# Kernel tuning notes

Measured on AMD Instinct MI355X. Metric: run time of the kernel, lower is better.

Reference implementation:

```python
import jax, jax.numpy as jnp
import numpy as np

E = 256; H = 8; HD = E // H
L_LEN = 300; A_LEN = 250
T = 768; B = 4
NEG = -1e9


def setup_inputs() -> dict:
    rng = jax.random.key(0)
    ks = jax.random.split(rng, 16)
    n = lambda k, s, sc=1.0: jax.random.normal(k, s, dtype=jnp.float32) * sc
    return {
        "query": n(ks[0], (T, B, E)),
        "key": n(ks[1], (T, B, E)),
        "value": n(ks[2], (T, B, E)),
        "in_proj_w": n(ks[3], (3 * E, E), 0.05),
        "in_proj_b": jnp.zeros((3 * E,), jnp.float32),
        "out_w": n(ks[4], (7, E, E), 0.05),
        "out_b": jnp.zeros((7, E), jnp.float32),
        "s_l_w": n(ks[5], (E, 4 * E), 0.05),
        "s_l_b": jnp.zeros((E,), jnp.float32),
        "s_a_w": n(ks[6], (E, 4 * E), 0.05),
        "s_a_b": jnp.zeros((E,), jnp.float32),
        "s_v_w": n(ks[7], (E, 4 * E), 0.05),
        "s_v_b": jnp.zeros((E,), jnp.float32),
        "final_w": n(ks[8], (E, E), 0.05),
        "final_b": jnp.zeros((E,), jnp.float32),
    }


def _forward(query, key, value, in_proj_w, in_proj_b, out_w, out_b,
             s_l_w, s_l_b, s_a_w, s_a_b, s_v_w, s_v_b, final_w, final_b):
    t, b, e = query.shape
    scaling = HD ** -0.5
    Wq, Wk, Wv = in_proj_w[:E], in_proj_w[E:2 * E], in_proj_w[2 * E:]
    bq, bk, bv = in_proj_b[:E], in_proj_b[E:2 * E], in_proj_b[2 * E:]
    q = (query @ Wq.T + bq) * scaling
    k = key @ Wk.T + bk
    v = value @ Wv.T + bv
    # (T, B, E) -> (B*H, T, HD)
    sh = lambda x: x.reshape(t, b * H, HD).transpose(1, 0, 2)
    q, k, v = sh(q), sh(k), sh(v)
    # shared QK^T, reused by all 7 masked branches
    scores = jnp.einsum('bth,bsh->bts', q, k)  # (B*H, T, T)
    idx = jnp.arange(t)
    seg = jnp.where(idx < L_LEN, 0, jnp.where(idx < L_LEN + A_LEN, 1, 2))

    def branch(i, mods):
        # m[j] = 1 iff position j belongs to one of the selected modalities
        m = sum((seg == s) for s in mods).astype(scores.dtype)  # (T,)
        # additive mask: in-set query attends only in-set keys; out-of-set
        # query rows get all -1e9 (uniform softmax, zeroed by row mask below)
        add = jnp.where((m[:, None] * m[None, :]) > 0, 0.0, NEG)
        w = jax.nn.softmax(scores + add, axis=-1) * m[None, :, None]
        o = jnp.einsum('bts,bsh->bth', w, v * m[None, :, None])
        o = o.transpose(1, 0, 2).reshape(t, b, e)
        return o @ out_w[i].T + out_b[i]

    attn_lav = branch(0, (0, 1, 2))
    attn_la = branch(1, (0, 1))
    attn_lv = branch(2, (0, 2))
    attn_av = branch(3, (1, 2))
    attn_l = branch(4, (0,))
    attn_a = branch(5, (1,))
    attn_v = branch(6, (2,))

    sl = jnp.concatenate([attn_lav, attn_la, attn_lv, attn_l], -1) @ s_l_w.T + s_l_b
    sa = jnp.concatenate([attn_lav, attn_la, attn_av, attn_a], -1) @ s_a_w.T + s_a_b
    sv = jnp.concatenate([attn_lav, attn_lv, attn_av, attn_v], -1) @ s_v_w.T + s_v_b
    return (sl + sa + sv) @ final_w.T + final_b


def reference(query, key, value, in_proj_w, in_proj_b, out_w, out_b,
              s_l_w, s_l_b, s_a_w, s_a_b, s_v_w, s_v_b, final_w, final_b):
    return _forward(query, key, value, in_proj_w, in_proj_b, out_w, out_b,
                    s_l_w, s_l_b, s_a_w, s_a_b, s_v_w, s_v_b, final_w, final_b)
```

## Files before the change

### kernel.cpp

```cpp
#include <hip/hip_runtime.h>
#include <hip/hip_bf16.h>

#define E 256
#define H 8
#define HD 32
#define T 768
#define B 4
#define BH 32

typedef __attribute__((ext_vector_type(8))) short bf16x8;
typedef __attribute__((ext_vector_type(4))) float f32x4;

__device__ __forceinline__ float b2f(__hip_bfloat16 x) { return __bfloat162float(x); }

__device__ __forceinline__ unsigned short f2bf_u(float x) {
    __hip_bfloat16 h = __float2bfloat16(x);
    return *(unsigned short*)&h;
}
__device__ __forceinline__ float bfu2f(unsigned short u) {
    return __uint_as_float(((unsigned int)u) << 16);
}

__device__ __forceinline__ void f8_split(const float* v, bf16x8& h, bf16x8& l) {
    #pragma unroll
    for (int e = 0; e < 8; ++e) {
        unsigned short hu = f2bf_u(v[e]);
        h[e] = (short)hu;
        l[e] = (short)f2bf_u(v[e] - bfu2f(hu));
    }
}

#define MFMA3(ACC, AH, AL, BH_, BL_)                                         \
    ACC = __builtin_amdgcn_mfma_f32_16x16x32_bf16(AH, BH_, ACC, 0, 0, 0);    \
    ACC = __builtin_amdgcn_mfma_f32_16x16x32_bf16(AH, BL_, ACC, 0, 0, 0);    \
    ACC = __builtin_amdgcn_mfma_f32_16x16x32_bf16(AL, BH_, ACC, 0, 0, 0);

__device__ __forceinline__ float ldu(const void* p, size_t i, int f32) {
    if (f32) return ((const float*)p)[i];
    return b2f(((const __hip_bfloat16*)p)[i]);
}

__device__ __forceinline__ float gsum_load(int i, int r2, int r,
                                           const void* sl, const void* sa,
                                           const void* sv, int f32)
{
    size_t base = (size_t)r2 * 1024;
    switch (i) {
        case 0: return ldu(sl, base + r, f32) + ldu(sa, base + r, f32) + ldu(sv, base + r, f32);
        case 1: return ldu(sl, base + 256 + r, f32) + ldu(sa, base + 256 + r, f32);
        case 2: return ldu(sl, base + 512 + r, f32) + ldu(sv, base + 256 + r, f32);
        case 3: return ldu(sa, base + 512 + r, f32) + ldu(sv, base + 512 + r, f32);
        case 4: return ldu(sl, base + 768 + r, f32);
        case 5: return ldu(sa, base + 768 + r, f32);
        default: return ldu(sv, base + 768 + r, f32);
    }
}

__global__ void detect_kernel(const unsigned short* __restrict__ q,
                              int* __restrict__ flag) {
    if (threadIdx.x == 0 && blockIdx.x == 0) {
        int f32 = 0;
        for (int i = 0; i < 256; ++i) {
            unsigned int bits = ((unsigned int)q[i]) << 16;
            float v = __uint_as_float(bits);
            if (!(v == v) || fabsf(v) > 1e4f) f32 = 1;
        }
        *flag = f32;
    }
}

__global__ __launch_bounds__(256) void conv_kernel(
    const void* query, const void* key, const void* value, const void* w,
    const void* sl, const void* sa, const void* sv, const void* outw,
    const int* __restrict__ flag,
    unsigned short* __restrict__ XFh, unsigned short* __restrict__ XFl,
    unsigned short* __restrict__ WFh, unsigned short* __restrict__ WFl,
    unsigned short* __restrict__ GFh, unsigned short* __restrict__ GFl,
    unsigned short* __restrict__ OWFh, unsigned short* __restrict__ OWFl)
{
    int f32 = *flag;
    int item = blockIdx.x * 256 + threadIdx.x;
    if (item < 294912) {
        int inp = item / 98304;
        int rem = item % 98304;
        int row = rem >> 5, kg = rem & 31;
        const void* X = (inp == 0) ? query : (inp == 1) ? key : value;
        float v[8];
        if (f32) {
            const float4* p = (const float4*)((const float*)X +
                               (size_t)row * 256 + kg * 8);
            *(float4*)&v[0] = p[0];
            *(float4*)&v[4] = p[1];
        } else {
            #pragma unroll
            for (int j = 0; j < 8; ++j)
                v[j] = ldu(X, (size_t)row * 256 + kg * 8 + j, 0);
        }
        bf16x8 h, l;
        f8_split(v, h, l);
        int rb = row >> 4, kb = kg >> 2;
        int lane = (row & 15) | ((kg & 3) << 4);
        size_t idx = (((size_t)(inp * 192 + rb) * 8 + kb) * 64 + lane) * 8;
        *(bf16x8*)&XFh[idx] = h;
        *(bf16x8*)&XFl[idx] = l;
    } else if (item < 319488) {
        int rem = item - 294912;
        int gc = rem >> 5, kg = rem & 31;
        float v[8];
        if (f32) {
            const float4* p = (const float4*)((const float*)w +
                               (size_t)gc * 256 + kg * 8);
            *(float4*)&v[0] = p[0];
            *(float4*)&v[4] = p[1];
        } else {
            #pragma unroll
            for (int j = 0; j < 8; ++j)
                v[j] = ldu(w, (size_t)gc * 256 + kg * 8 + j, 0);
        }
        bf16x8 h, l;
        f8_split(v, h, l);
        int sec = gc >> 8, c = gc & 255;
        int cb = c >> 4, kb = kg >> 2;
        int lane = (c & 15) | ((kg & 3) << 4);
        size_t idx = (((size_t)(sec * 16 + cb) * 8 + kb) * 64 + lane) * 8;
        *(bf16x8*)&WFh[idx] = h;
        *(bf16x8*)&WFl[idx] = l;
    } else if (item < 376832) {
        int rem = item - 319488;
        int i = rem >> 13;
        int rest = rem & 8191;
        int r2 = rest >> 5, kg = rest & 31;
        float v[8];
        #pragma unroll
        for (int j = 0; j < 8; ++j)
            v[j] = gsum_load(i, r2, kg * 8 + j, sl, sa, sv, f32);
        bf16x8 h, l;
        f8_split(v, h, l);
        int rb = r2 >> 4, kb = kg >> 2;
        int lane = (r2 & 15) | ((kg & 3) << 4);
        size_t idx = (((size_t)(i * 16 + rb) * 8 + kb) * 64 + lane) * 8;
        *(bf16x8*)&GFh[idx] = h;
        *(bf16x8*)&GFl[idx] = l;
    } else if (item < 434176) {
        int rem = item - 376832;
        int i = rem >> 13;
        int rest = rem & 8191;
        int kg = rest >> 8, c = rest & 255;
        float v[8];
        #pragma unroll
        for (int j = 0; j < 8; ++j)
            v[j] = ldu(outw, (size_t)i * 65536 + (kg * 8 + j) * 256 + c, f32);
        bf16x8 h, l;
        f8_split(v, h, l);
        int cb = c >> 4, kb = kg >> 2;
        int lane = (c & 15) | ((kg & 3) << 4);
        size_t idx = (((size_t)(i * 16 + cb) * 8 + kb) * 64 + lane) * 8;
        *(bf16x8*)&OWFh[idx] = h;
        *(bf16x8*)&OWFl[idx] = l;
    }
}

__global__ __launch_bounds__(256) void qkv_mfma_kernel(
    const unsigned short* __restrict__ XFh, const unsigned short* __restrict__ XFl,
    const unsigned short* __restrict__ WFh, const unsigned short* __restrict__ WFl,
    const void* bias, const int* __restrict__ flag,
    float* __restrict__ qws,
    unsigned short* __restrict__ KGh, unsigned short* __restrict__ KGl,
    unsigned short* __restrict__ VGh, unsigned short* __restrict__ VGl)
{
    int f32 = *flag;
    int bx = blockIdx.x;
    int rb = blockIdx.y;
    int sec = bx >> 2, cg = bx & 3;
    int w = threadIdx.x >> 6, lane = threadIdx.x & 63;
    int m = lane & 15, quad = lane >> 4;
    int cb = cg * 4 + w;

    const unsigned short* Ah = XFh + (((size_t)(sec * 192 + rb) * 8) * 64 + lane) * 8;
    const unsigned short* Al = XFl + (((size_t)(sec * 192 + rb) * 8) * 64 + lane) * 8;
    const unsigned short* Bh = WFh + (((size_t)(sec * 16 + cb) * 8) * 64 + lane) * 8;
    const unsigned short* Bl = WFl + (((size_t)(sec * 16 + cb) * 8) * 64 + lane) * 8;

    f32x4 acc = {};
    #pragma unroll
    for (int kb = 0; kb < 8; ++kb) {
        size_t off = (size_t)kb * 512;
        bf16x8 ah = *(const bf16x8*)(Ah + off);
        bf16x8 al = *(const bf16x8*)(Al + off);
        bf16x8 bh = *(const bf16x8*)(Bh + off);
        bf16x8 bl = *(const bf16x8*)(Bl + off);
        MFMA3(acc, ah, al, bh, bl)
    }

    int c_local = cb * 16 + m;
    float bv = ldu(bias, sec * 256 + c_local, f32);
    int h = c_local >> 5, hd = c_local & 31;

    if (sec == 0) {
        #pragma unroll
        for (int rr = 0; rr < 4; ++rr) {
            int row = rb * 16 + quad * 4 + rr;
            int t = row >> 2, b = row & 3;
            float val = (acc[rr] + bv) * 0.17677669529663687f;
            qws[((size_t)((b * H + h) * T + t)) * HD + hd] = val;
        }
    } else if (sec == 1) {
        #pragma unroll
        for (int rr = 0; rr < 4; ++rr) {
            int row = rb * 16 + quad * 4 + rr;
            int s = row >> 2, b = row & 3;
            int bh_ = b * 8 + h, ch = s >> 6;
            float val = acc[rr] + bv;
            unsigned short hu = f2bf_u(val);
            unsigned short lu = f2bf_u(val - bfu2f(hu));
            size_t bi = (((size_t)(bh_ * 12 + ch) * 4 + ((s >> 4) & 3)) * 64
                         + ((s & 15) | ((hd >> 3) << 4))) * 8 + (hd & 7);
            KGh[bi] = hu;
            KGl[bi] = lu;
        }
    } else {
        #pragma unroll
        for (int rr = 0; rr < 4; ++rr) {
            int row = rb * 16 + quad * 4 + rr;
            int s = row >> 2, b = row & 3;
            int bh_ = b * 8 + h, ch = s >> 6;
            float val = acc[rr] + bv;
            unsigned short hu = f2bf_u(val);
            unsigned short lu = f2bf_u(val - bfu2f(hu));
            int sl = s & 63, ks = sl >> 5, j = sl & 7, q3 = (sl >> 3) & 3;
            int hdb = hd >> 4;
            size_t bi = ((((size_t)(bh_ * 12 + ch) * 2 + hdb) * 2 + ks) * 64
                         + ((hd & 15) | (q3 << 4))) * 8 + j;
            VGh[bi] = hu;
            VGl[bi] = lu;
        }
    }
}

__global__ __launch_bounds__(256) void wcomb1_mfma_kernel(
    const unsigned short* __restrict__ GFh, const unsigned short* __restrict__ GFl,
    const unsigned short* __restrict__ OWFh, const unsigned short* __restrict__ OWFl,
    float* __restrict__ Mtmp)
{
    int cgrp = blockIdx.x;
    int rb   = blockIdx.y;
    int i    = blockIdx.z;
    int w = threadIdx.x >> 6, lane = threadIdx.x & 63;
    int m = lane & 15, quad = lane >> 4;
    int cb = cgrp * 4 + w;

    const unsigned short* Ah = GFh + (((size_t)(i * 16 + rb) * 8) * 64 + lane) * 8;
    const unsigned short* Al = GFl + (((size_t)(i * 16 + rb) * 8) * 64 + lane) * 8;
    const unsigned short* Bh = OWFh + (((size_t)(i * 16 + cb) * 8) * 64 + lane) * 8;
    const unsigned short* Bl = OWFl + (((size_t)(i * 16 + cb) * 8) * 64 + lane) * 8;

    f32x4 acc = {};
    #pragma unroll
    for (int kb = 0; kb < 8; ++kb) {
        size_t off = (size_t)kb * 512;
        bf16x8 ah = *(const bf16x8*)(Ah + off);
        bf16x8 al = *(const bf16x8*)(Al + off);
        bf16x8 bh = *(const bf16x8*)(Bh + off);
        bf16x8 bl = *(const bf16x8*)(Bl + off);
        MFMA3(acc, ah, al, bh, bl)
    }
    #pragma unroll
    for (int rr = 0; rr < 4; ++rr) {
        int r2 = rb * 16 + quad * 4 + rr;
        Mtmp[(size_t)i * 65536 + r2 * 256 + cb * 16 + m] = acc[rr];
    }
}

__global__ __launch_bounds__(256) void attn_mfma_kernel(
    const float* __restrict__ qws,
    const unsigned short* __restrict__ KGh, const unsigned short* __restrict__ KGl,
    const unsigned short* __restrict__ VGh, const unsigned short* __restrict__ VGl,
    unsigned short* __restrict__ Ohi, unsigned short* __restrict__ Olo)
{
    int tile = blockIdx.x;
    int bh   = blockIdx.y;
    int t0 = tile * 32;
    int tid = threadIdx.x;
    int w = tid >> 6, lane = tid & 63;
    int m = lane & 15, quad = lane >> 4;
    int tb = w & 1, hdb = w >> 1;

    __shared__ __align__(16) unsigned int EPK[2][2048];
    __shared__ float SP[4][16][3];
    float* PL = (float*)&EPK[0][0];

    bf16x8 aqh, aql;
    {
        const float* qr = qws + ((size_t)bh * T + t0 + tb * 16 + m) * HD + quad * 8;
        float qv[8];
        *(float4*)&qv[0] = *(const float4*)qr;
        *(float4*)&qv[4] = *(const float4*)(qr + 4);
        f8_split(qv, aqh, aql);
    }

    f32x4 acc0 = {}, acc1 = {}, acc2 = {};
    float ss0[4] = {}, ss1[4] = {}, ss2[4] = {};

    for (int ch = 0; ch < 12; ++ch) {
        int base = ch * 64;
        int buf = ch & 1;
        #pragma unroll
        for (int sbi = 0; sbi < 2; ++sbi) {
            int sb = (w >> 1) * 2 + sbi;
            size_t kfi = (((size_t)(bh * 12 + ch) * 4 + sb) * 64 + lane) * 8;
            bf16x8 bkh = *(const bf16x8*)(KGh + kfi);
            bf16x8 bkl = *(const bf16x8*)(KGl + kfi);
            f32x4 d = {};
            MFMA3(d, aqh, aql, bkh, bkl)
            int s64 = sb * 16 + m;
            int sglob = base + s64;
            int ksw = s64 >> 5, qp = (s64 >> 3) & 3, jp = m & 7;
            unsigned int* eb = &EPK[buf][(tb * 2 + ksw) * 512 + jp];
            #pragma unroll
            for (int r = 0; r < 4; ++r) {
                float e = __expf(d[r]);
                if (sglob < 300) ss0[r] += e;
                else if (sglob < 550) ss1[r] += e;
                else ss2[r] += e;
                unsigned short hu = f2bf_u(e);
                unsigned short lu = f2bf_u(e - bfu2f(hu));
                eb[((quad * 4 + r) + 16 * qp) * 8] =
                    (unsigned int)hu | ((unsigned int)lu << 16);
            }
        }
        __syncthreads();

        #pragma unroll
        for (int ks = 0; ks < 2; ++ks) {
            const unsigned int* ep = &EPK[buf][((tb * 2 + ks) * 64 + lane) * 8];
            uint4 p0 = *(const uint4*)ep;
            uint4 p1 = *(const uint4*)(ep + 4);
            bf16x8 aeh, ael;
            aeh[0] = (short)(p0.x & 0xffff); ael[0] = (short)(p0.x >> 16);
            aeh[1] = (short)(p0.y & 0xffff); ael[1] = (short)(p0.y >> 16);
            aeh[2] = (short)(p0.z & 0xffff); ael[2] = (short)(p0.z >> 16);
            aeh[3] = (short)(p0.w & 0xffff); ael[3] = (short)(p0.w >> 16);
            aeh[4] = (short)(p1.x & 0xffff); ael[4] = (short)(p1.x >> 16);
            aeh[5] = (short)(p1.y & 0xffff); ael[5] = (short)(p1.y >> 16);
            aeh[6] = (short)(p1.z & 0xffff); ael[6] = (short)(p1.z >> 16);
            aeh[7] = (short)(p1.w & 0xffff); ael[7] = (short)(p1.w >> 16);
            size_t vfi = ((((size_t)(bh * 12 + ch) * 2 + hdb) * 2 + ks) * 64 + lane) * 8;
            bf16x8 bvh = *(const bf16x8*)(VGh + vfi);
            bf16x8 bvl = *(const bf16x8*)(VGl + vfi);
            int s_lo = base + ks * 32;
            if (s_lo + 32 <= 300) { MFMA3(acc0, aeh, ael, bvh, bvl) }
            else if (s_lo >= 300 && s_lo + 32 <= 550) { MFMA3(acc1, aeh, ael, bvh, bvl) }
            else if (s_lo >= 550) { MFMA3(acc2, aeh, ael, bvh, bvl) }
            else {
                int bnd = (s_lo < 300) ? 300 : 550;
                bf16x8 eha = aeh, ela = ael, ehb = aeh, elb = ael;
                #pragma unroll
                for (int j = 0; j < 8; ++j) {
                    int s = s_lo + quad * 8 + j;
                    if (s < bnd) { ehb[j] = 0; elb[j] = 0; }
                    else         { eha[j] = 0; ela[j] = 0; }
                }
                if (s_lo < 300) { MFMA3(acc0, eha, ela, bvh, bvl)
                                  MFMA3(acc1, ehb, elb, bvh, bvl) }
                else            { MFMA3(acc1, eha, ela, bvh, bvl)
                                  MFMA3(acc2, ehb, elb, bvh, bvl) }
            }
        }
    }

    #pragma unroll
    for (int sg = 0; sg < 3; ++sg)
        #pragma unroll
        for (int r = 0; r < 4; ++r) {
            float v = (sg == 0) ? ss0[r] : (sg == 1) ? ss1[r] : ss2[r];
            v += __shfl_down(v, 8, 16);
            v += __shfl_down(v, 4, 16);
            v += __shfl_down(v, 2, 16);
            v += __shfl_down(v, 1, 16);
            if (m == 0) SP[w][quad * 4 + r][sg] = v;
        }
    __syncthreads();

    #pragma unroll
    for (int r = 0; r < 4; ++r) {
        int t32 = tb * 16 + quad * 4 + r;
        int hd = hdb * 16 + m;
        PL[0 * 1152 + t32 * 36 + hd] = acc0[r];
        PL[1 * 1152 + t32 * 36 + hd] = acc1[r];
        PL[2 * 1152 + t32 * 36 + hd] = acc2[r];
    }
    __syncthreads();

    int tt = tid >> 3, q4 = tid & 7;
    float Pv[3][4];
    #pragma unroll
    for (int sg = 0; sg < 3; ++sg) {
        const float4 p = *(const float4*)&PL[sg * 1152 + tt * 36 + q4 * 4];
        Pv[sg][0] = p.x; Pv[sg][1] = p.y; Pv[sg][2] = p.z; Pv[sg][3] = p.w;
    }
    int tbe = tt >> 4, t16 = tt & 15;
    float S0 = SP[tbe][t16][0] + SP[tbe + 2][t16][0];
    float S1 = SP[tbe][t16][1] + SP[tbe + 2][t16][1];
    float S2 = SP[tbe][t16][2] + SP[tbe + 2][t16][2];

    int t_glob = t0 + tt;
    int g = (t_glob < 300) ? 0 : (t_glob < 550 ? 1 : 2);
    int b_ = bh >> 3, h_ = bh & 7;
    int row = t_glob * B + b_;
    int lslot = (row & 15) + ((q4 >> 1) << 4);
    int j0 = (q4 & 1) * 4;
    size_t fbase = (((size_t)(row >> 4) * 56 + h_) * 64 + lslot) * 8 + j0;
    const int masks[7] = {7, 3, 5, 6, 1, 2, 4};
    #pragma unroll
    for (int i = 0; i < 7; ++i) {
        int mm = masks[i];
        float n0 = 0.f, n1 = 0.f, n2 = 0.f, n3 = 0.f, den = 0.f;
        if (mm & 1) { n0 += Pv[0][0]; n1 += Pv[0][1]; n2 += Pv[0][2]; n3 += Pv[0][3]; den += S0; }
        if (mm & 2) { n0 += Pv[1][0]; n1 += Pv[1][1]; n2 += Pv[1][2]; n3 += Pv[1][3]; den += S1; }
        if (mm & 4) { n0 += Pv[2][0]; n1 += Pv[2][1]; n2 += Pv[2][2]; n3 += Pv[2][3]; den += S2; }
        float r = 1.f / den;
        int live = (mm >> g) & 1;
        float o[4];
        o[0] = live ? n0 * r : 0.f;
        o[1] = live ? n1 * r : 0.f;
        o[2] = live ? n2 * r : 0.f;
        o[3] = live ? n3 * r : 0.f;
        ushort4 hi4, lo4;
        unsigned short* hp = (unsigned short*)&hi4;
        unsigned short* lp = (unsigned short*)&lo4;
        #pragma unroll
        for (int j = 0; j < 4; ++j) {
            unsigned short hu = f2bf_u(o[j]);
            hp[j] = hu;
            lp[j] = f2bf_u(o[j] - bfu2f(hu));
        }
        size_t addr = fbase + (size_t)i * (8 * 64 * 8);
        *(ushort4*)&Ohi[addr] = hi4;
        *(ushort4*)&Olo[addr] = lo4;
    }
}

__global__ __launch_bounds__(256) void wcomb2_gemm_kernel(
    const float* __restrict__ Mtmp, const void* finalw,
    const int* __restrict__ flag,
    unsigned short* __restrict__ DThi, unsigned short* __restrict__ DTlo)
{
    int f32 = *flag;
    int bx = blockIdx.x;
    int by = blockIdx.y;
    int i  = blockIdx.z;
    int tid = threadIdx.x;
    int tx = tid & 15, ty = tid >> 4;
    int colbase = bx * 32, rowbase = by * 32;
    __shared__ __align__(16) float AsT[32][34];
    __shared__ __align__(16) float Bs[32][34];
    float acc[2][2] = {};

    for (int kb = 0; kb < 8; ++kb) {
        __syncthreads();
        #pragma unroll
        for (int l = 0; l < 4; ++l) {
            int idx = l * 256 + tid;
            int c = idx & 31, kk = idx >> 5;
            AsT[kk][c] = Mtmp[(size_t)i * 65536 + (kb * 32 + kk) * 256 + rowbase + c];
            int k2 = idx & 31, n = idx >> 5;
            Bs[k2][n] = ldu(finalw, (size_t)(colbase + n) * 256 + kb * 32 + k2, f32);
        }
        __syncthreads();
        #pragma unroll 8
        for (int kk = 0; kk < 32; ++kk) {
            const float2 av = *(const float2*)&AsT[kk][ty * 2];
            const float2 bv = *(const float2*)&Bs[kk][tx * 2];
            acc[0][0] += av.x * bv.x; acc[0][1] += av.x * bv.y;
            acc[1][0] += av.y * bv.x; acc[1][1] += av.y * bv.y;
        }
    }
    #pragma unroll
    for (int u = 0; u < 2; ++u)
        #pragma unroll
        for (int v = 0; v < 2; ++v) {
            int c = rowbase + ty * 2 + u, e = colbase + tx * 2 + v;
            float a = acc[u][v];
            unsigned short hu = f2bf_u(a);
            size_t fidx = (((size_t)(e >> 4) * 56 + i * 8 + (c >> 5)) * 64
                           + (e & 15) + (((c >> 3) & 3) << 4)) * 8 + (c & 7);
            DThi[fidx] = hu;
            DTlo[fidx] = f2bf_u(a - bfu2f(hu));
        }
}

__global__ __launch_bounds__(256) void bias1_kernel(
    const void* sl, const void* sa, const void* sv, const void* outb,
    const void* slb, const void* sab, const void* svb,
    const int* __restrict__ flag, float* __restrict__ c0)
{
    int f32 = *flag;
    int r2 = blockIdx.x, m = threadIdx.x;
    __shared__ float red[256];
    float acc = 0.f;
    #pragma unroll
    for (int i = 0; i < 7; ++i)
        acc += ldu(outb, i * 256 + m, f32) * gsum_load(i, r2, m, sl, sa, sv, f32);
    red[m] = acc;
    __syncthreads();
    for (int s = 128; s > 0; s >>= 1) {
        if (m < s) red[m] += red[m + s];
        __syncthreads();
    }
    if (m == 0)
        c0[r2] = red[0] + ldu(slb, r2, f32) + ldu(sab, r2, f32) + ldu(svb, r2, f32);
}

__global__ __launch_bounds__(256) void bias2_kernel(
    const float* __restrict__ c0, const void* finalw, const void* finalb,
    const int* __restrict__ flag, float* __restrict__ d0)
{
    int f32 = *flag;
    int e = blockIdx.x, r = threadIdx.x;
    __shared__ float red[256];
    red[r] = c0[r] * ldu(finalw, (size_t)e * 256 + r, f32);
    __syncthreads();
    for (int s = 128; s > 0; s >>= 1) {
        if (r < s) red[r] += red[r + s];
        __syncthreads();
    }
    if (r == 0)
        d0[e] = red[0] + ldu(finalb, e, f32);
}

__global__ __launch_bounds__(256) void final_gemm_mfma_kernel(
    const unsigned short* __restrict__ Ohi, const unsigned short* __restrict__ Olo,
    const unsigned short* __restrict__ DThi, const unsigned short* __restrict__ DTlo,
    const float* __restrict__ d0, const int* __restrict__ flag,
    void* __restrict__ outv)
{
    int f32 = *flag;
    int bx = blockIdx.x;
    int by = blockIdx.y;
    int w  = threadIdx.x >> 6;
    int lane = threadIdx.x & 63;
    int m = lane & 15, quad = lane >> 4;
    int R0 = by * 16, C0 = bx * 64 + w * 16;

    int t0 = R0 >> 2, t1 = (R0 + 15) >> 2;
    int g0 = (t0 < 300) ? 0 : (t0 < 550 ? 1 : 2);
    int g1 = (t1 < 300) ? 0 : (t1 < 550 ? 1 : 2);
    int activeset = (1 << g0) | (1 << g1);
    const int masks[7] = {7, 3, 5, 6, 1, 2, 4};

    const unsigned short* Abase_h = Ohi + (size_t)by * 56 * 512 + lane * 8;
    const unsigned short* Abase_l = Olo + (size_t)by * 56 * 512 + lane * 8;
    const unsigned short* Bbase_h = DThi + (size_t)(bx * 4 + w) * 56 * 512 + lane * 8;
    const unsigned short* Bbase_l = DTlo + (size_t)(bx * 4 + w) * 56 * 512 + lane * 8;

    f32x4 acc = {};
    for (int i = 0; i < 7; ++i) {
        if (!(masks[i] & activeset)) continue;
        #pragma unroll
        for (int kb = 0; kb < 8; ++kb) {
            size_t off = (size_t)(i * 8 + kb) * 512;
            bf16x8 ah = *(const bf16x8*)(Abase_h + off);
            bf16x8 al = *(const bf16x8*)(Abase_l + off);
            bf16x8 bh = *(const bf16x8*)(Bbase_h + off);
            bf16x8 bl = *(const bf16x8*)(Bbase_l + off);
            acc = __builtin_amdgcn_mfma_f32_16x16x32_bf16(ah, bh, acc, 0, 0, 0);
            acc = __builtin_amdgcn_mfma_f32_16x16x32_bf16(ah, bl, acc, 0, 0, 0);
            acc = __builtin_amdgcn_mfma_f32_16x16x32_bf16(al, bh, acc, 0, 0, 0);
        }
    }
    float dv = d0[C0 + m];
    #pragma unroll
    for (int r = 0; r < 4; ++r) {
        int row = R0 + quad * 4 + r;
        int col = C0 + m;
        float val = acc[r] + dv;
        if (f32) ((float*)outv)[(size_t)row * 256 + col] = val;
        else ((__hip_bfloat16*)outv)[(size_t)row * 256 + col] = __float2bfloat16(val);
    }
}

extern "C" void kernel_launch(void* const* d_in, const int* in_sizes, int n_in,
                              void* d_out, int out_size, void* d_ws, size_t ws_size,
                              hipStream_t stream) {
    const void* query     = d_in[0];
    const void* key       = d_in[1];
    const void* value     = d_in[2];
    const void* in_proj_w = d_in[3];
    const void* in_proj_b = d_in[4];
    const void* out_w     = d_in[5];
    const void* out_b     = d_in[6];
    const void* s_l_w     = d_in[7];
    const void* s_l_b     = d_in[8];
    const void* s_a_w     = d_in[9];
    const void* s_a_b     = d_in[10];
    const void* s_v_w     = d_in[11];
    const void* s_v_b     = d_in[12];
    const void* final_w   = d_in[13];
    const void* final_b   = d_in[14];

    float* ws     = (float*)d_ws;
    float* qws    = ws;
    unsigned short* KGh = (unsigned short*)(ws + 786432);
    unsigned short* KGl = KGh + 786432;
    unsigned short* VGh = (unsigned short*)(ws + 1572864);
    unsigned short* VGl = VGh + 786432;
    unsigned short* Ohi = (unsigned short*)(ws + 2359296);
    unsigned short* Olo = (unsigned short*)(ws + 5111808);
    unsigned short* XFh = (unsigned short*)(ws + 2359296);
    unsigned short* XFl = XFh + 2359296;
    unsigned short* WFh = XFl + 2359296;
    unsigned short* WFl = WFh + 196608;
    unsigned short* GFh = (unsigned short*)(ws + 4915200);
    unsigned short* GFl = GFh + 458752;
    unsigned short* OWFh = GFl + 458752;
    unsigned short* OWFl = OWFh + 458752;
    float* Mtmp   = ws + 7864320;
    unsigned short* DThi = (unsigned short*)(ws + 8323072);
    unsigned short* DTlo = (unsigned short*)(ws + 8552448);
    float* d0     = ws + 8781824;
    int*   flag   = (int*)(ws + 8782080);
    float* c0     = Mtmp;

    detect_kernel<<<1, 64, 0, stream>>>((const unsigned short*)query, flag);
    conv_kernel<<<1696, 256, 0, stream>>>(query, key, value, in_proj_w,
                                          s_l_w, s_a_w, s_v_w, out_w, flag,
                                          XFh, XFl, WFh, WFl,
                                          GFh, GFl, OWFh, OWFl);
    qkv_mfma_kernel<<<dim3(12, 192), 256, 0, stream>>>(XFh, XFl, WFh, WFl,
                                                       in_proj_b, flag, qws,
                                                       KGh, KGl, VGh, VGl);
    wcomb1_mfma_kernel<<<dim3(4, 16, 7), 256, 0, stream>>>(GFh, GFl, OWFh, OWFl,
                                                           Mtmp);
    attn_mfma_kernel<<<dim3(24, 32), 256, 0, stream>>>(qws, KGh, KGl, VGh, VGl,
                                                       Ohi, Olo);
    wcomb2_gemm_kernel<<<dim3(8, 8, 7), 256, 0, stream>>>(Mtmp, final_w, flag,
                                                          DThi, DTlo);
    bias1_kernel<<<256, 256, 0, stream>>>(s_l_w, s_a_w, s_v_w, out_b,
                                          s_l_b, s_a_b, s_v_b, flag, c0);
    bias2_kernel<<<256, 256, 0, stream>>>(c0, final_w, final_b, flag, d0);
    final_gemm_mfma_kernel<<<dim3(4, 192), 256, 0, stream>>>(Ohi, Olo, DThi, DTlo,
                                                             d0, flag, d_out);
}
```

Measured before the change: 198.3 us.

## Split attention key loop across two blocks and combine partials in a new kernel

The attention kernel now splits its 12 key chunks into two halves across a new grid z dimension, doubling the block count from 768 to 1536 to fill more CUs. Each half writes unnormalized PV accumulators and row exp-sums to global scratch buffers. A new combine kernel sums the two partials and does the per-branch normalization and the bf16 hi/lo output packing. This trades extra global traffic and an additional launch for more parallelism. It relies on the softmax not subtracting a running max, so partial sums can be added directly.

Result: slower. 207.1 us (+4.4%).

```diff
diff --git a/kernel.cpp b/kernel.cpp
--- a/kernel.cpp
+++ b/kernel.cpp
@@ -275,10 +275,11 @@
     const float* __restrict__ qws,
     const unsigned short* __restrict__ KGh, const unsigned short* __restrict__ KGl,
     const unsigned short* __restrict__ VGh, const unsigned short* __restrict__ VGl,
-    unsigned short* __restrict__ Ohi, unsigned short* __restrict__ Olo)
+    float* __restrict__ PACC, float* __restrict__ PSUM)
 {
     int tile = blockIdx.x;
     int bh   = blockIdx.y;
+    int z    = blockIdx.z;
     int t0 = tile * 32;
     int tid = threadIdx.x;
     int w = tid >> 6, lane = tid & 63;
@@ -287,7 +288,6 @@
 
     __shared__ __align__(16) unsigned int EPK[2][2048];
     __shared__ float SP[4][16][3];
-    float* PL = (float*)&EPK[0][0];
 
     bf16x8 aqh, aql;
     {
@@ -301,7 +301,7 @@
     f32x4 acc0 = {}, acc1 = {}, acc2 = {};
     float ss0[4] = {}, ss1[4] = {}, ss2[4] = {};
 
-    for (int ch = 0; ch < 12; ++ch) {
+    for (int ch = z * 6; ch < z * 6 + 6; ++ch) {
         int base = ch * 64;
         int buf = ch & 1;
         #pragma unroll
@@ -381,29 +381,45 @@
         }
     __syncthreads();
 
+    size_t pb = ((((size_t)z * 24 + tile) * 32 + bh) * 3) * 1024;
     #pragma unroll
     for (int r = 0; r < 4; ++r) {
-        int t32 = tb * 16 + quad * 4 + r;
-        int hd = hdb * 16 + m;
-        PL[0 * 1152 + t32 * 36 + hd] = acc0[r];
-        PL[1 * 1152 + t32 * 36 + hd] = acc1[r];
-        PL[2 * 1152 + t32 * 36 + hd] = acc2[r];
-    }
-    __syncthreads();
-
+        int idx = (tb * 16 + quad * 4 + r) * 32 + hdb * 16 + m;
+        PACC[pb + idx]        = acc0[r];
+        PACC[pb + 1024 + idx] = acc1[r];
+        PACC[pb + 2048 + idx] = acc2[r];
+    }
+    if (tid < 96) {
+        int sg = tid >> 5, t32 = tid & 31;
+        int tbe = t32 >> 4, t16 = t32 & 15;
+        PSUM[(((size_t)z * 24 + tile) * 32 + bh) * 96 + sg * 32 + t32] =
+            SP[tbe][t16][sg] + SP[tbe + 2][t16][sg];
+    }
+}
+
+__global__ __launch_bounds__(256) void attn_combine_kernel(
+    const float* __restrict__ PACC, const float* __restrict__ PSUM,
+    unsigned short* __restrict__ Ohi, unsigned short* __restrict__ Olo)
+{
+    int tile = blockIdx.x;
+    int bh   = blockIdx.y;
+    int tid = threadIdx.x;
     int tt = tid >> 3, q4 = tid & 7;
-    float Pv[3][4];
+
+    size_t p0 = (((size_t)0 * 24 + tile) * 32 + bh) * 3072;
+    size_t p1 = (((size_t)1 * 24 + tile) * 32 + bh) * 3072;
+    float Pv[3][4], S[3];
     #pragma unroll
     for (int sg = 0; sg < 3; ++sg) {
-        const float4 p = *(const float4*)&PL[sg * 1152 + tt * 36 + q4 * 4];
-        Pv[sg][0] = p.x; Pv[sg][1] = p.y; Pv[sg][2] = p.z; Pv[sg][3] = p.w;
-    }
-    int tbe = tt >> 4, t16 = tt & 15;
-    float S0 = SP[tbe][t16][0] + SP[tbe + 2][t16][0];
-    float S1 = SP[tbe][t16][1] + SP[tbe + 2][t16][1];
-    float S2 = SP[tbe][t16][2] + SP[tbe + 2][t16][2];
-
-    int t_glob = t0 + tt;
+        const float4 a = *(const float4*)&PACC[p0 + sg * 1024 + tt * 32 + q4 * 4];
+        const float4 b = *(const float4*)&PACC[p1 + sg * 1024 + tt * 32 + q4 * 4];
+        Pv[sg][0] = a.x + b.x; Pv[sg][1] = a.y + b.y;
+        Pv[sg][2] = a.z + b.z; Pv[sg][3] = a.w + b.w;
+        S[sg] = PSUM[((size_t)tile * 32 + bh) * 96 + sg * 32 + tt]
+              + PSUM[((size_t)(24 + tile) * 32 + bh) * 96 + sg * 32 + tt];
+    }
+
+    int t_glob = tile * 32 + tt;
     int g = (t_glob < 300) ? 0 : (t_glob < 550 ? 1 : 2);
     int b_ = bh >> 3, h_ = bh & 7;
     int row = t_glob * B + b_;
@@ -415,9 +431,9 @@
     for (int i = 0; i < 7; ++i) {
         int mm = masks[i];
         float n0 = 0.f, n1 = 0.f, n2 = 0.f, n3 = 0.f, den = 0.f;
-        if (mm & 1) { n0 += Pv[0][0]; n1 += Pv[0][1]; n2 += Pv[0][2]; n3 += Pv[0][3]; den += S0; }
-        if (mm & 2) { n0 += Pv[1][0]; n1 += Pv[1][1]; n2 += Pv[1][2]; n3 += Pv[1][3]; den += S1; }
-        if (mm & 4) { n0 += Pv[2][0]; n1 += Pv[2][1]; n2 += Pv[2][2]; n3 += Pv[2][3]; den += S2; }
+        if (mm & 1) { n0 += Pv[0][0]; n1 += Pv[0][1]; n2 += Pv[0][2]; n3 += Pv[0][3]; den += S[0]; }
+        if (mm & 2) { n0 += Pv[1][0]; n1 += Pv[1][1]; n2 += Pv[1][2]; n3 += Pv[1][3]; den += S[1]; }
+        if (mm & 4) { n0 += Pv[2][0]; n1 += Pv[2][1]; n2 += Pv[2][2]; n3 += Pv[2][3]; den += S[2]; }
         float r = 1.f / den;
         int live = (mm >> g) & 1;
         float o[4];
@@ -620,6 +636,8 @@
     float* d0     = ws + 8781824;
     int*   flag   = (int*)(ws + 8782080);
     float* c0     = Mtmp;
+    float* PACC   = ws + 8782336;
+    float* PSUM   = ws + 13500928;
 
     detect_kernel<<<1, 64, 0, stream>>>((const unsigned short*)query, flag);
     conv_kernel<<<1696, 256, 0, stream>>>(query, key, value, in_proj_w,
@@ -631,8 +649,9 @@
                                                        KGh, KGl, VGh, VGl);
     wcomb1_mfma_kernel<<<dim3(4, 16, 7), 256, 0, stream>>>(GFh, GFl, OWFh, OWFl,
                                                            Mtmp);
-    attn_mfma_kernel<<<dim3(24, 32), 256, 0, stream>>>(qws, KGh, KGl, VGh, VGl,
-                                                       Ohi, Olo);
+    attn_mfma_kernel<<<dim3(24, 32, 2), 256, 0, stream>>>(qws, KGh, KGl, VGh, VGl,
+                                                          PACC, PSUM);
+    attn_combine_kernel<<<dim3(24, 32), 256, 0, stream>>>(PACC, PSUM, Ohi, Olo);
     wcomb2_gemm_kernel<<<dim3(8, 8, 7), 256, 0, stream>>>(Mtmp, final_w, flag,
                                                           DThi, DTlo);
     bias1_kernel<<<256, 256, 0, stream>>>(s_l_w, s_a_w, s_v_w, out_b,
```

## Prefetch next K/V chunk into registers and swizzle LDS exp buffer

Applied to the files above, without the earlier changes.

The attention kernel now loads the next chunk's K and V MFMA fragments into registers while the current chunk is computed, which hides global load latency behind the exp and MFMA work. The LDS writes and reads of the packed exp values use an XOR swizzle to reduce bank conflicts. Launch bounds now request three blocks per CU, and the chunk loop is unrolled by two. The extra prefetch registers could raise register pressure or cause spills under the occupancy hint.

Measured after the change: 194.8 us. No clear change (-1.8%).

```diff
diff --git a/kernel.cpp b/kernel.cpp
--- a/kernel.cpp
+++ b/kernel.cpp
@@ -271,7 +271,7 @@
     }
 }
 
-__global__ __launch_bounds__(256) void attn_mfma_kernel(
+__global__ __launch_bounds__(256, 3) void attn_mfma_kernel(
     const float* __restrict__ qws,
     const unsigned short* __restrict__ KGh, const unsigned short* __restrict__ KGl,
     const unsigned short* __restrict__ VGh, const unsigned short* __restrict__ VGl,
@@ -301,21 +301,44 @@
     f32x4 acc0 = {}, acc1 = {}, acc2 = {};
     float ss0[4] = {}, ss1[4] = {}, ss2[4] = {};
 
+    int sb0 = (w >> 1) * 2;
+
+    bf16x8 ckh0, ckl0, ckh1, ckl1, cvh0, cvl0, cvh1, cvl1;
+    {
+        size_t k0 = (((size_t)(bh * 12 + 0) * 4 + sb0) * 64 + lane) * 8;
+        ckh0 = *(const bf16x8*)(KGh + k0);       ckl0 = *(const bf16x8*)(KGl + k0);
+        ckh1 = *(const bf16x8*)(KGh + k0 + 512); ckl1 = *(const bf16x8*)(KGl + k0 + 512);
+        size_t v0 = ((((size_t)(bh * 12 + 0) * 2 + hdb) * 2) * 64 + lane) * 8;
+        cvh0 = *(const bf16x8*)(VGh + v0);       cvl0 = *(const bf16x8*)(VGl + v0);
+        cvh1 = *(const bf16x8*)(VGh + v0 + 512); cvl1 = *(const bf16x8*)(VGl + v0 + 512);
+    }
+
+    #pragma unroll 2
     for (int ch = 0; ch < 12; ++ch) {
         int base = ch * 64;
         int buf = ch & 1;
+
+        bf16x8 nkh0, nkl0, nkh1, nkl1, nvh0, nvl0, nvh1, nvl1;
+        if (ch < 11) {
+            size_t kn = (((size_t)(bh * 12 + ch + 1) * 4 + sb0) * 64 + lane) * 8;
+            nkh0 = *(const bf16x8*)(KGh + kn);       nkl0 = *(const bf16x8*)(KGl + kn);
+            nkh1 = *(const bf16x8*)(KGh + kn + 512); nkl1 = *(const bf16x8*)(KGl + kn + 512);
+            size_t vn = ((((size_t)(bh * 12 + ch + 1) * 2 + hdb) * 2) * 64 + lane) * 8;
+            nvh0 = *(const bf16x8*)(VGh + vn);       nvl0 = *(const bf16x8*)(VGl + vn);
+            nvh1 = *(const bf16x8*)(VGh + vn + 512); nvl1 = *(const bf16x8*)(VGl + vn + 512);
+        }
+
         #pragma unroll
         for (int sbi = 0; sbi < 2; ++sbi) {
-            int sb = (w >> 1) * 2 + sbi;
-            size_t kfi = (((size_t)(bh * 12 + ch) * 4 + sb) * 64 + lane) * 8;
-            bf16x8 bkh = *(const bf16x8*)(KGh + kfi);
-            bf16x8 bkl = *(const bf16x8*)(KGl + kfi);
+            bf16x8 bkh = sbi ? ckh1 : ckh0;
+            bf16x8 bkl = sbi ? ckl1 : ckl0;
             f32x4 d = {};
             MFMA3(d, aqh, aql, bkh, bkl)
+            int sb = sb0 + sbi;
             int s64 = sb * 16 + m;
             int sglob = base + s64;
             int ksw = s64 >> 5, qp = (s64 >> 3) & 3, jp = m & 7;
-            unsigned int* eb = &EPK[buf][(tb * 2 + ksw) * 512 + jp];
+            int wbase = (tb * 2 + ksw) * 512 + jp;
             #pragma unroll
             for (int r = 0; r < 4; ++r) {
                 float e = __expf(d[r]);
@@ -324,17 +347,21 @@
                 else ss2[r] += e;
                 unsigned short hu = f2bf_u(e);
                 unsigned short lu = f2bf_u(e - bfu2f(hu));
-                eb[((quad * 4 + r) + 16 * qp) * 8] =
-                    (unsigned int)hu | ((unsigned int)lu << 16);
+                int wi = wbase + ((quad * 4 + r) + 16 * qp) * 8;
+                wi ^= ((wi >> 5) & 7) << 2;
+                EPK[buf][wi] = (unsigned int)hu | ((unsigned int)lu << 16);
             }
         }
         __syncthreads();
 
         #pragma unroll
         for (int ks = 0; ks < 2; ++ks) {
-            const unsigned int* ep = &EPK[buf][((tb * 2 + ks) * 64 + lane) * 8];
-            uint4 p0 = *(const uint4*)ep;
-            uint4 p1 = *(const uint4*)(ep + 4);
+            int ri = (tb * 2 + ks) * 512 + lane * 8;
+            int rs = ri ^ (((ri >> 5) & 7) << 2);
+            const unsigned int* e0 = &EPK[buf][rs];
+            const unsigned int* e1 = &EPK[buf][rs ^ 4];
+            uint4 p0 = *(const uint4*)e0;
+            uint4 p1 = *(const uint4*)e1;
             bf16x8 aeh, ael;
             aeh[0] = (short)(p0.x & 0xffff); ael[0] = (short)(p0.x >> 16);
             aeh[1] = (short)(p0.y & 0xffff); ael[1] = (short)(p0.y >> 16);
@@ -344,9 +371,8 @@
             aeh[5] = (short)(p1.y & 0xffff); ael[5] = (short)(p1.y >> 16);
             aeh[6] = (short)(p1.z & 0xffff); ael[6] = (short)(p1.z >> 16);
             aeh[7] = (short)(p1.w & 0xffff); ael[7] = (short)(p1.w >> 16);
-            size_t vfi = ((((size_t)(bh * 12 + ch) * 2 + hdb) * 2 + ks) * 64 + lane) * 8;
-            bf16x8 bvh = *(const bf16x8*)(VGh + vfi);
-            bf16x8 bvl = *(const bf16x8*)(VGl + vfi);
+            bf16x8 bvh = ks ? cvh1 : cvh0;
+            bf16x8 bvl = ks ? cvl1 : cvl0;
             int s_lo = base + ks * 32;
             if (s_lo + 32 <= 300) { MFMA3(acc0, aeh, ael, bvh, bvl) }
             else if (s_lo >= 300 && s_lo + 32 <= 550) { MFMA3(acc1, aeh, ael, bvh, bvl) }
@@ -365,6 +391,11 @@
                 else            { MFMA3(acc1, eha, ela, bvh, bvl)
                                   MFMA3(acc2, ehb, elb, bvh, bvl) }
             }
+        }
+
+        if (ch < 11) {
+            ckh0 = nkh0; ckl0 = nkl0; ckh1 = nkh1; ckl1 = nkl1;
+            cvh0 = nvh0; cvl0 = nvl0; cvh1 = nvh1; cvl1 = nvl1;
         }
     }
 
```

## Restructure attention to 32x32 MFMA with register-resident P and per-wave key split

Applied to the files above, without the earlier changes.

The attention kernel moves from 16x16x32 to 32x32x16 bf16 MFMAs and computes S^T = K·Q^T, so the exponentiated probabilities stay in registers and are redistributed with a cross-half shuffle instead of an LDS round trip with a barrier every chunk. Each wave now owns three 64-key chunks rather than all waves sweeping every chunk together, and partial accumulators and row sums are reduced across waves through shared memory once at the end. K and V are written in plain row-major and transposed layouts to suit the new fragment loads. Launch bounds request 3 blocks per SIMD. In exchange the segment-boundary masking becomes hard-coded per chunk, and there are 32-wide accumulators and a more complex final reduction.

Measured after the change: 199.3 us. No clear change (+0.5%).

```diff
diff --git a/kernel.cpp b/kernel.cpp
--- a/kernel.cpp
+++ b/kernel.cpp
@@ -10,6 +10,7 @@
 
 typedef __attribute__((ext_vector_type(8))) short bf16x8;
 typedef __attribute__((ext_vector_type(4))) float f32x4;
+typedef __attribute__((ext_vector_type(16))) float f32x16;
 
 __device__ __forceinline__ float b2f(__hip_bfloat16 x) { return __bfloat162float(x); }
 
@@ -34,6 +35,17 @@
     ACC = __builtin_amdgcn_mfma_f32_16x16x32_bf16(AH, BH_, ACC, 0, 0, 0);    \
     ACC = __builtin_amdgcn_mfma_f32_16x16x32_bf16(AH, BL_, ACC, 0, 0, 0);    \
     ACC = __builtin_amdgcn_mfma_f32_16x16x32_bf16(AL, BH_, ACC, 0, 0, 0);
+
+#define MFMA3W(ACC, AH, AL, BH_, BL_)                                        \
+    ACC = __builtin_amdgcn_mfma_f32_32x32x16_bf16(AH, BH_, ACC, 0, 0, 0);    \
+    ACC = __builtin_amdgcn_mfma_f32_32x32x16_bf16(AH, BL_, ACC, 0, 0, 0);    \
+    ACC = __builtin_amdgcn_mfma_f32_32x32x16_bf16(AL, BH_, ACC, 0, 0, 0);
+
+__device__ __forceinline__ bf16x8 mk8(int a, int b, int c, int d) {
+    union { int i[4]; bf16x8 v; } u;
+    u.i[0] = a; u.i[1] = b; u.i[2] = c; u.i[3] = d;
+    return u.v;
+}
 
 __device__ __forceinline__ float ldu(const void* p, size_t i, int f32) {
     if (f32) return ((const float*)p)[i];
@@ -165,8 +177,8 @@
     const unsigned short* __restrict__ WFh, const unsigned short* __restrict__ WFl,
     const void* bias, const int* __restrict__ flag,
     float* __restrict__ qws,
-    unsigned short* __restrict__ KGh, unsigned short* __restrict__ KGl,
-    unsigned short* __restrict__ VGh, unsigned short* __restrict__ VGl)
+    unsigned short* __restrict__ KRh, unsigned short* __restrict__ KRl,
+    unsigned short* __restrict__ VTh, unsigned short* __restrict__ VTl)
 {
     int f32 = *flag;
     int bx = blockIdx.x;
@@ -209,30 +221,26 @@
         for (int rr = 0; rr < 4; ++rr) {
             int row = rb * 16 + quad * 4 + rr;
             int s = row >> 2, b = row & 3;
-            int bh_ = b * 8 + h, ch = s >> 6;
+            int bh_ = b * 8 + h;
             float val = acc[rr] + bv;
             unsigned short hu = f2bf_u(val);
             unsigned short lu = f2bf_u(val - bfu2f(hu));
-            size_t bi = (((size_t)(bh_ * 12 + ch) * 4 + ((s >> 4) & 3)) * 64
-                         + ((s & 15) | ((hd >> 3) << 4))) * 8 + (hd & 7);
-            KGh[bi] = hu;
-            KGl[bi] = lu;
+            size_t bi = ((size_t)bh_ * 768 + s) * 32 + hd;
+            KRh[bi] = hu;
+            KRl[bi] = lu;
         }
     } else {
         #pragma unroll
         for (int rr = 0; rr < 4; ++rr) {
             int row = rb * 16 + quad * 4 + rr;
             int s = row >> 2, b = row & 3;
-            int bh_ = b * 8 + h, ch = s >> 6;
+            int bh_ = b * 8 + h;
             float val = acc[rr] + bv;
             unsigned short hu = f2bf_u(val);
             unsigned short lu = f2bf_u(val - bfu2f(hu));
-            int sl = s & 63, ks = sl >> 5, j = sl & 7, q3 = (sl >> 3) & 3;
-            int hdb = hd >> 4;
-            size_t bi = ((((size_t)(bh_ * 12 + ch) * 2 + hdb) * 2 + ks) * 64
-                         + ((hd & 15) | (q3 << 4))) * 8 + j;
-            VGh[bi] = hu;
-            VGl[bi] = lu;
+            size_t bi = ((size_t)bh_ * 32 + hd) * 768 + s;
+            VTh[bi] = hu;
+            VTl[bi] = lu;
         }
     }
 }
@@ -271,10 +279,10 @@
     }
 }
 
-__global__ __launch_bounds__(256) void attn_mfma_kernel(
+__global__ __launch_bounds__(256, 3) void attn_mfma_kernel(
     const float* __restrict__ qws,
-    const unsigned short* __restrict__ KGh, const unsigned short* __restrict__ KGl,
-    const unsigned short* __restrict__ VGh, const unsigned short* __restrict__ VGl,
+    const unsigned short* __restrict__ KRh, const unsigned short* __restrict__ KRl,
+    const unsigned short* __restrict__ VTh, const unsigned short* __restrict__ VTl,
     unsigned short* __restrict__ Ohi, unsigned short* __restrict__ Olo)
 {
     int tile = blockIdx.x;
@@ -282,126 +290,176 @@
     int t0 = tile * 32;
     int tid = threadIdx.x;
     int w = tid >> 6, lane = tid & 63;
-    int m = lane & 15, quad = lane >> 4;
-    int tb = w & 1, hdb = w >> 1;
-
-    __shared__ __align__(16) unsigned int EPK[2][2048];
-    __shared__ float SP[4][16][3];
-    float* PL = (float*)&EPK[0][0];
-
-    bf16x8 aqh, aql;
+    int ln = lane & 31, h = lane >> 5;
+
+    __shared__ float AC2[2][3][32][36];
+    __shared__ float SS2[2][3][32];
+
+    bf16x8 qbh[2], qbl[2];
     {
-        const float* qr = qws + ((size_t)bh * T + t0 + tb * 16 + m) * HD + quad * 8;
-        float qv[8];
-        *(float4*)&qv[0] = *(const float4*)qr;
-        *(float4*)&qv[4] = *(const float4*)(qr + 4);
-        f8_split(qv, aqh, aql);
-    }
-
-    f32x4 acc0 = {}, acc1 = {}, acc2 = {};
-    float ss0[4] = {}, ss1[4] = {}, ss2[4] = {};
-
-    for (int ch = 0; ch < 12; ++ch) {
-        int base = ch * 64;
-        int buf = ch & 1;
-        #pragma unroll
-        for (int sbi = 0; sbi < 2; ++sbi) {
-            int sb = (w >> 1) * 2 + sbi;
-            size_t kfi = (((size_t)(bh * 12 + ch) * 4 + sb) * 64 + lane) * 8;
-            bf16x8 bkh = *(const bf16x8*)(KGh + kfi);
-            bf16x8 bkl = *(const bf16x8*)(KGl + kfi);
-            f32x4 d = {};
-            MFMA3(d, aqh, aql, bkh, bkl)
-            int s64 = sb * 16 + m;
-            int sglob = base + s64;
-            int ksw = s64 >> 5, qp = (s64 >> 3) & 3, jp = m & 7;
-            unsigned int* eb = &EPK[buf][(tb * 2 + ksw) * 512 + jp];
+        const float* qr = qws + ((size_t)bh * T + t0 + ln) * HD + h * 8;
+        #pragma unroll
+        for (int c = 0; c < 2; ++c) {
+            float qv[8];
+            *(float4*)&qv[0] = *(const float4*)(qr + c * 16);
+            *(float4*)&qv[4] = *(const float4*)(qr + c * 16 + 4);
+            f8_split(qv, qbh[c], qbl[c]);
+        }
+    }
+
+    f32x16 accA = {}, accB = {};
+    float ssA = 0.f, ssB = 0.f;
+
+    for (int q = 0; q < 3; ++q) {
+        int ch = w * 3 + q;
+        int sbase = ch * 64;
+        int route = (ch == 5) ? 1 : (ch == 4 || ch == 8) ? 2 : 0;
+        int bnd = (ch == 4) ? 300 : 550;
+        bool c12 = (ch == 4);
+
+        int PH[2][8], PL[2][8];
+        #pragma unroll
+        for (int st = 0; st < 2; ++st) {
+            size_t krow = ((size_t)bh * 768 + sbase + st * 32 + ln) * 32 + h * 8;
+            bf16x8 kh0 = *(const bf16x8*)(KRh + krow);
+            bf16x8 kl0 = *(const bf16x8*)(KRl + krow);
+            bf16x8 kh1 = *(const bf16x8*)(KRh + krow + 16);
+            bf16x8 kl1 = *(const bf16x8*)(KRl + krow + 16);
+            f32x16 d = {};
+            MFMA3W(d, kh0, kl0, qbh[0], qbl[0])
+            MFMA3W(d, kh1, kl1, qbh[1], qbl[1])
+
+            int EH[16], EL[16];
             #pragma unroll
-            for (int r = 0; r < 4; ++r) {
+            for (int r = 0; r < 16; ++r) {
                 float e = __expf(d[r]);
-                if (sglob < 300) ss0[r] += e;
-                else if (sglob < 550) ss1[r] += e;
-                else ss2[r] += e;
-                unsigned short hu = f2bf_u(e);
-                unsigned short lu = f2bf_u(e - bfu2f(hu));
-                eb[((quad * 4 + r) + 16 * qp) * 8] =
-                    (unsigned int)hu | ((unsigned int)lu << 16);
+                if (route == 2) {
+                    int s = sbase + st * 32 + (r & 3) + 8 * (r >> 2) + 4 * h;
+                    if (s < bnd) ssA += e; else ssB += e;
+                } else if (route == 1) ssB += e;
+                else ssA += e;
+                unsigned int eb = __float_as_uint(e);
+                float lo = e - __uint_as_float(eb & 0xffff0000u);
+                EH[r] = (int)eb;
+                EL[r] = (int)__float_as_uint(lo);
             }
-        }
-        __syncthreads();
-
-        #pragma unroll
-        for (int ks = 0; ks < 2; ++ks) {
-            const unsigned int* ep = &EPK[buf][((tb * 2 + ks) * 64 + lane) * 8];
-            uint4 p0 = *(const uint4*)ep;
-            uint4 p1 = *(const uint4*)(ep + 4);
-            bf16x8 aeh, ael;
-            aeh[0] = (short)(p0.x & 0xffff); ael[0] = (short)(p0.x >> 16);
-            aeh[1] = (short)(p0.y & 0xffff); ael[1] = (short)(p0.y >> 16);
-            aeh[2] = (short)(p0.z & 0xffff); ael[2] = (short)(p0.z >> 16);
-            aeh[3] = (short)(p0.w & 0xffff); ael[3] = (short)(p0.w >> 16);
-            aeh[4] = (short)(p1.x & 0xffff); ael[4] = (short)(p1.x >> 16);
-            aeh[5] = (short)(p1.y & 0xffff); ael[5] = (short)(p1.y >> 16);
-            aeh[6] = (short)(p1.z & 0xffff); ael[6] = (short)(p1.z >> 16);
-            aeh[7] = (short)(p1.w & 0xffff); ael[7] = (short)(p1.w >> 16);
-            size_t vfi = ((((size_t)(bh * 12 + ch) * 2 + hdb) * 2 + ks) * 64 + lane) * 8;
-            bf16x8 bvh = *(const bf16x8*)(VGh + vfi);
-            bf16x8 bvl = *(const bf16x8*)(VGl + vfi);
-            int s_lo = base + ks * 32;
-            if (s_lo + 32 <= 300) { MFMA3(acc0, aeh, ael, bvh, bvl) }
-            else if (s_lo >= 300 && s_lo + 32 <= 550) { MFMA3(acc1, aeh, ael, bvh, bvl) }
-            else if (s_lo >= 550) { MFMA3(acc2, aeh, ael, bvh, bvl) }
+            #pragma unroll
+            for (int p = 0; p < 8; ++p) {
+                PH[st][p] = (int)(((unsigned)EH[2*p] >> 16) |
+                                  ((unsigned)EH[2*p+1] & 0xffff0000u));
+                PL[st][p] = (int)(((unsigned)EL[2*p] >> 16) |
+                                  ((unsigned)EL[2*p+1] & 0xffff0000u));
+            }
+        }
+
+        #pragma unroll
+        for (int ks = 0; ks < 4; ++ks) {
+            int st = ks >> 1, cc = 4 * (ks & 1);
+            size_t vrow = ((size_t)bh * 32 + ln) * 768 + sbase + ks * 16 + h * 8;
+            bf16x8 vbh = *(const bf16x8*)(VTh + vrow);
+            bf16x8 vbl = *(const bf16x8*)(VTl + vrow);
+
+            int sh0 = __shfl_xor(PH[st][cc+0], 32);
+            int sh1 = __shfl_xor(PH[st][cc+1], 32);
+            int sh2 = __shfl_xor(PH[st][cc+2], 32);
+            int sh3 = __shfl_xor(PH[st][cc+3], 32);
+            int sl0 = __shfl_xor(PL[st][cc+0], 32);
+            int sl1 = __shfl_xor(PL[st][cc+1], 32);
+            int sl2 = __shfl_xor(PL[st][cc+2], 32);
+            int sl3 = __shfl_xor(PL[st][cc+3], 32);
+            int FH0 = h ? sh2 : PH[st][cc+0];
+            int FH1 = h ? sh3 : PH[st][cc+1];
+            int FH2 = h ? PH[st][cc+2] : sh0;
+            int FH3 = h ? PH[st][cc+3] : sh1;
+            int FL0 = h ? sl2 : PL[st][cc+0];
+            int FL1 = h ? sl3 : PL[st][cc+1];
+            int FL2 = h ? PL[st][cc+2] : sl0;
+            int FL3 = h ? PL[st][cc+3] : sl1;
+            bf16x8 feh = mk8(FH0, FH1, FH2, FH3);
+            bf16x8 fel = mk8(FL0, FL1, FL2, FL3);
+
+            if (route == 0)      { MFMA3W(accA, feh, fel, vbh, vbl) }
+            else if (route == 1) { MFMA3W(accB, feh, fel, vbh, vbl) }
             else {
-                int bnd = (s_lo < 300) ? 300 : 550;
-                bf16x8 eha = aeh, ela = ael, ehb = aeh, elb = ael;
-                #pragma unroll
-                for (int j = 0; j < 8; ++j) {
-                    int s = s_lo + quad * 8 + j;
-                    if (s < bnd) { ehb[j] = 0; elb[j] = 0; }
-                    else         { eha[j] = 0; ela[j] = 0; }
+                if (ks < 2)       { MFMA3W(accA, feh, fel, vbh, vbl) }
+                else if (ks == 3) { MFMA3W(accB, feh, fel, vbh, vbl) }
+                else {
+                    int a0 = h ? (c12 ? FH0 : 0) : FH0;
+                    int a1 = h ? (c12 ? FH1 : 0) : FH1;
+                    int a2 = h ? 0 : FH2;
+                    int a3 = h ? 0 : (c12 ? FH3 : 0);
+                    int b0 = h ? (c12 ? 0 : FH0) : 0;
+                    int b1 = h ? (c12 ? 0 : FH1) : 0;
+                    int b2 = h ? FH2 : 0;
+                    int b3 = h ? FH3 : (c12 ? 0 : FH3);
+                    int la0 = h ? (c12 ? FL0 : 0) : FL0;
+                    int la1 = h ? (c12 ? FL1 : 0) : FL1;
+                    int la2 = h ? 0 : FL2;
+                    int la3 = h ? 0 : (c12 ? FL3 : 0);
+                    int lb0 = h ? (c12 ? 0 : FL0) : 0;
+                    int lb1 = h ? (c12 ? 0 : FL1) : 0;
+                    int lb2 = h ? FL2 : 0;
+                    int lb3 = h ? FL3 : (c12 ? 0 : FL3);
+                    bf16x8 fha = mk8(a0, a1, a2, a3), fla = mk8(la0, la1, la2, la3);
+                    bf16x8 fhb = mk8(b0, b1, b2, b3), flb = mk8(lb0, lb1, lb2, lb3);
+                    MFMA3W(accA, fha, fla, vbh, vbl)
+                    MFMA3W(accB, fhb, flb, vbh, vbl)
                 }
-                if (s_lo < 300) { MFMA3(acc0, eha, ela, bvh, bvl)
-                                  MFMA3(acc1, ehb, elb, bvh, bvl) }
-                else            { MFMA3(acc1, eha, ela, bvh, bvl)
-                                  MFMA3(acc2, ehb, elb, bvh, bvl) }
             }
         }
     }
 
-    #pragma unroll
-    for (int sg = 0; sg < 3; ++sg)
-        #pragma unroll
-        for (int r = 0; r < 4; ++r) {
-            float v = (sg == 0) ? ss0[r] : (sg == 1) ? ss1[r] : ss2[r];
-            v += __shfl_down(v, 8, 16);
-            v += __shfl_down(v, 4, 16);
-            v += __shfl_down(v, 2, 16);
-            v += __shfl_down(v, 1, 16);
-            if (m == 0) SP[w][quad * 4 + r][sg] = v;
-        }
+    ssA += __shfl_xor(ssA, 32);
+    ssB += __shfl_xor(ssB, 32);
+
+    int bsel = w & 1;
+    f32x16 zz = {};
+    f32x16 o0 = (w <= 1) ? accA : zz;
+    f32x16 o1 = (w == 1) ? accB : (w == 2) ? accA : zz;
+    f32x16 o2 = (w == 2) ? accB : (w == 3) ? accA : zz;
+    float s0 = (w <= 1) ? ssA : 0.f;
+    float s1 = (w == 1) ? ssB : (w == 2) ? ssA : 0.f;
+    float s2 = (w == 2) ? ssB : (w == 3) ? ssA : 0.f;
+
+    if (w < 2) {
+        #pragma unroll
+        for (int r = 0; r < 16; ++r) {
+            int t = (r & 3) + 8 * (r >> 2) + 4 * h;
+            AC2[bsel][0][t][ln] = o0[r];
+            AC2[bsel][1][t][ln] = o1[r];
+            AC2[bsel][2][t][ln] = o2[r];
+        }
+        if (h == 0) {
+            SS2[bsel][0][ln] = s0;
+            SS2[bsel][1][ln] = s1;
+            SS2[bsel][2][ln] = s2;
+        }
+    }
     __syncthreads();
-
-    #pragma unroll
-    for (int r = 0; r < 4; ++r) {
-        int t32 = tb * 16 + quad * 4 + r;
-        int hd = hdb * 16 + m;
-        PL[0 * 1152 + t32 * 36 + hd] = acc0[r];
-        PL[1 * 1152 + t32 * 36 + hd] = acc1[r];
-        PL[2 * 1152 + t32 * 36 + hd] = acc2[r];
+    if (w >= 2) {
+        #pragma unroll
+        for (int r = 0; r < 16; ++r) {
+            int t = (r & 3) + 8 * (r >> 2) + 4 * h;
+            AC2[bsel][1][t][ln] += o1[r];
+            AC2[bsel][2][t][ln] += o2[r];
+        }
+        if (h == 0) {
+            SS2[bsel][1][ln] += s1;
+            SS2[bsel][2][ln] += s2;
+        }
     }
     __syncthreads();
 
     int tt = tid >> 3, q4 = tid & 7;
-    float Pv[3][4];
+    float Pv[3][4], S[3];
     #pragma unroll
     for (int sg = 0; sg < 3; ++sg) {
-        const float4 p = *(const float4*)&PL[sg * 1152 + tt * 36 + q4 * 4];
-        Pv[sg][0] = p.x; Pv[sg][1] = p.y; Pv[sg][2] = p.z; Pv[sg][3] = p.w;
-    }
-    int tbe = tt >> 4, t16 = tt & 15;
-    float S0 = SP[tbe][t16][0] + SP[tbe + 2][t16][0];
-    float S1 = SP[tbe][t16][1] + SP[tbe + 2][t16][1];
-    float S2 = SP[tbe][t16][2] + SP[tbe + 2][t16][2];
+        const float4 a = *(const float4*)&AC2[0][sg][tt][q4 * 4];
+        const float4 b = *(const float4*)&AC2[1][sg][tt][q4 * 4];
+        Pv[sg][0] = a.x + b.x; Pv[sg][1] = a.y + b.y;
+        Pv[sg][2] = a.z + b.z; Pv[sg][3] = a.w + b.w;
+        S[sg] = SS2[0][sg][tt] + SS2[1][sg][tt];
+    }
 
     int t_glob = t0 + tt;
     int g = (t_glob < 300) ? 0 : (t_glob < 550 ? 1 : 2);
@@ -415,9 +473,9 @@
     for (int i = 0; i < 7; ++i) {
         int mm = masks[i];
         float n0 = 0.f, n1 = 0.f, n2 = 0.f, n3 = 0.f, den = 0.f;
-        if (mm & 1) { n0 += Pv[0][0]; n1 += Pv[0][1]; n2 += Pv[0][2]; n3 += Pv[0][3]; den += S0; }
-        if (mm & 2) { n0 += Pv[1][0]; n1 += Pv[1][1]; n2 += Pv[1][2]; n3 += Pv[1][3]; den += S1; }
-        if (mm & 4) { n0 += Pv[2][0]; n1 += Pv[2][1]; n2 += Pv[2][2]; n3 += Pv[2][3]; den += S2; }
+        if (mm & 1) { n0 += Pv[0][0]; n1 += Pv[0][1]; n2 += Pv[0][2]; n3 += Pv[0][3]; den += S[0]; }
+        if (mm & 2) { n0 += Pv[1][0]; n1 += Pv[1][1]; n2 += Pv[1][2]; n3 += Pv[1][3]; den += S[1]; }
+        if (mm & 4) { n0 += Pv[2][0]; n1 += Pv[2][1]; n2 += Pv[2][2]; n3 += Pv[2][3]; den += S[2]; }
         float r = 1.f / den;
         int live = (mm >> g) & 1;
         float o[4];
@@ -600,10 +658,10 @@
 
     float* ws     = (float*)d_ws;
     float* qws    = ws;
-    unsigned short* KGh = (unsigned short*)(ws + 786432);
-    unsigned short* KGl = KGh + 786432;
-    unsigned short* VGh = (unsigned short*)(ws + 1572864);
-    unsigned short* VGl = VGh + 786432;
+    unsigned short* KRh = (unsigned short*)(ws + 786432);
+    unsigned short* KRl = KRh + 786432;
+    unsigned short* VTh = (unsigned short*)(ws + 1572864);
+    unsigned short* VTl = VTh + 786432;
     unsigned short* Ohi = (unsigned short*)(ws + 2359296);
     unsigned short* Olo = (unsigned short*)(ws + 5111808);
     unsigned short* XFh = (unsigned short*)(ws + 2359296);
@@ -628,10 +686,10 @@
                                           GFh, GFl, OWFh, OWFl);
     qkv_mfma_kernel<<<dim3(12, 192), 256, 0, stream>>>(XFh, XFl, WFh, WFl,
                                                        in_proj_b, flag, qws,
-                                                       KGh, KGl, VGh, VGl);
+                                                       KRh, KRl, VTh, VTl);
     wcomb1_mfma_kernel<<<dim3(4, 16, 7), 256, 0, stream>>>(GFh, GFl, OWFh, OWFl,
                                                            Mtmp);
-    attn_mfma_kernel<<<dim3(24, 32), 256, 0, stream>>>(qws, KGh, KGl, VGh, VGl,
+    attn_mfma_kernel<<<dim3(24, 32), 256, 0, stream>>>(qws, KRh, KRl, VTh, VTl,
                                                        Ohi, Olo);
     wcomb2_gemm_kernel<<<dim3(8, 8, 7), 256, 0, stream>>>(Mtmp, final_w, flag,
                                                           DThi, DTlo);
```
